# Performance work log

Measured on AMD Instinct MI355X. Metric: run time of the kernel, lower is better.

Reference implementation:

```python
import jax, jax.numpy as jnp
import numpy as np

E, D_IN, D_OUT, T = 8, 2048, 8192, 16384


def setup_inputs() -> dict:
    key = jax.random.key(0)
    k1, k2 = jax.random.split(key, 2)
    inp = jax.random.normal(k1, (T, D_IN), dtype=jnp.float32)
    # kaiming-uniform-ish scale for weight [E, d_out, d_in]
    bound = float(1.0 / np.sqrt(D_IN))
    weight = jax.random.uniform(k2, (E, D_OUT, D_IN), dtype=jnp.float32,
                                minval=-bound, maxval=bound)
    bias = jnp.zeros((E, D_OUT), dtype=jnp.float32)
    # tokens are pre-sorted by expert; equal load here (2048 tokens/expert)
    fwd_expert_count = jnp.full((E,), T // E, dtype=jnp.int32)
    return {"inp": inp, "fwd_expert_count": fwd_expert_count,
            "weight": weight, "bias": bias}


def reference(inp, fwd_expert_count, weight, bias):
    # Grouped GEMM: expert e processes the contiguous slab of
    # fwd_expert_count[e] rows of inp; y = x_e @ W[e].T + b[e].
    counts = np.asarray(fwd_expert_count)          # concrete host ints
    offsets = np.concatenate([[0], np.cumsum(counts)])
    outs = []
    for e in range(counts.shape[0]):
        x_e = inp[offsets[e]:offsets[e + 1]]        # [c_e, d_in]
        outs.append(x_e @ weight[e].T + bias[e])    # [c_e, d_out]
    return jnp.concatenate(outs, axis=0)            # [T, d_out]
```

## Files before the change

### kernel.cpp

```cpp
#include <hip/hip_runtime.h>
#include <stdint.h>

typedef unsigned short u16;
typedef __attribute__((ext_vector_type(8))) short short8;
typedef __attribute__((ext_vector_type(4))) float f32x4;

#define NE   8
#define DIN  2048
#define DOUT 8192
#define NTOK 16384

__device__ __forceinline__ u16 f2bf(float f) {
  uint32_t u = __builtin_bit_cast(uint32_t, f);
  u += 0x7FFFu + ((u >> 16) & 1u);
  return (u16)(u >> 16);
}

__global__ __launch_bounds__(256) void cvt_f32_bf16(const float* __restrict__ src,
                                                    u16* __restrict__ dst, size_t n) {
  size_t i = ((size_t)blockIdx.x * 256 + threadIdx.x) * 8;
  const size_t stride = (size_t)gridDim.x * 256 * 8;
  for (; i < n; i += stride) {
    f32x4 a = *(const f32x4*)(src + i);
    f32x4 b = *(const f32x4*)(src + i + 4);
    short8 o;
    o[0] = (short)f2bf(a[0]); o[1] = (short)f2bf(a[1]);
    o[2] = (short)f2bf(a[2]); o[3] = (short)f2bf(a[3]);
    o[4] = (short)f2bf(b[0]); o[5] = (short)f2bf(b[1]);
    o[6] = (short)f2bf(b[2]); o[7] = (short)f2bf(b[3]);
    *(short8*)(dst + i) = o;
  }
}

#define GLOAD_LDS16(g, l) __builtin_amdgcn_global_load_lds( \
    (const __attribute__((address_space(1))) void*)(g),     \
    (__attribute__((address_space(3))) void*)(l), 16, 0, 0)

__global__ __launch_bounds__(512, 2) void moe_gemm8(
    const u16* __restrict__ Xb, const u16* __restrict__ Wb,
    const int* __restrict__ counts, const float* __restrict__ bias,
    float* __restrict__ C) {
  extern __shared__ u16 sm[];

  const int tid = threadIdx.x;
  const int l = tid & 63;
  const int wid = tid >> 6;
  const int wr = wid >> 2;
  const int wc = wid & 3;

  const int id = blockIdx.x;
  const int swz = (id & 7) * 256 + (id >> 3);
  const int e = swz >> 8;
  const int rem = swz & 255;
  const int tn = rem >> 3;
  const int tm = rem & 7;

  int off = 0;
  for (int i = 0; i < e; ++i) off += counts[i];
  const int row0 = off + tm * 256;
  const int col0 = tn * 256;
  const size_t wbase = (size_t)e * DOUT * DIN + (size_t)col0 * DIN;

  const int rl = l >> 2;
  const int q = (l & 3) ^ ((l >> 3) & 3);
  const int s0 = wid * 2, s1 = s0 + 1;
  const u16* pA0 = Xb + (size_t)(row0 + s0 * 16 + rl) * DIN + q * 8;
  const u16* pA1 = Xb + (size_t)(row0 + s1 * 16 + rl) * DIN + q * 8;
  const u16* pB0 = Wb + wbase + (size_t)(s0 * 16 + rl) * DIN + q * 8;
  const u16* pB1 = Wb + wbase + (size_t)(s1 * 16 + rl) * DIN + q * 8;

  const int f0 = ((l & 15) >> 1) & 3;
  const int gph = (l >> 4) ^ f0;
  const int aoff = (wr * 128 + (l & 15)) * 32 + gph * 8;
  const int boff = (wc * 64 + (l & 15)) * 32 + gph * 8;

  f32x4 acc[8][4] = {};
  short8 a[4], b[4];

#define SMA(buf, kh) (sm + (buf) * 32768 + (kh) * 8192)
#define SMB(buf, kh) (sm + (buf) * 32768 + 16384 + (kh) * 8192)
#define STAGE_A(buf, kt, kh) do { const int ko = (kt) * 64 + (kh) * 32; \
    GLOAD_LDS16(pA0 + ko, SMA(buf, kh) + s0 * 512);                     \
    GLOAD_LDS16(pA1 + ko, SMA(buf, kh) + s1 * 512); } while (0)
#define STAGE_B(buf, kt, kh) do { const int ko = (kt) * 64 + (kh) * 32; \
    GLOAD_LDS16(pB0 + ko, SMB(buf, kh) + s0 * 512);                     \
    GLOAD_LDS16(pB1 + ko, SMB(buf, kh) + s1 * 512); } while (0)
#define RA4(buf, kh, mb) do { _Pragma("unroll") for (int mf = 0; mf < 4; ++mf) \
    a[mf] = *(const short8*)(SMA(buf, kh) + aoff + ((mb) + mf) * 512); } while (0)
#define RB4(buf, kh) do { _Pragma("unroll") for (int nf = 0; nf < 4; ++nf) \
    b[nf] = *(const short8*)(SMB(buf, kh) + boff + nf * 512); } while (0)
#define FENCE() asm volatile("" ::: "memory")
#define BAR() do { FENCE(); __builtin_amdgcn_s_barrier(); FENCE(); } while (0)
#define VMW(N) asm volatile("s_waitcnt vmcnt(" #N ")" ::: "memory")
#define LGKM0() asm volatile("s_waitcnt lgkmcnt(0)" ::: "memory")
#define MMQ(mb) do { __builtin_amdgcn_s_setprio(1);                                \
    _Pragma("unroll") for (int mf = 0; mf < 4; ++mf)                               \
      _Pragma("unroll") for (int nf = 0; nf < 4; ++nf)                             \
        acc[(mb) + mf][nf] =                                                       \
          __builtin_amdgcn_mfma_f32_16x16x32_bf16(a[mf], b[nf], acc[(mb) + mf][nf], 0, 0, 0); \
    __builtin_amdgcn_s_setprio(0); } while (0)

  const int NKT = DIN / 64;

  STAGE_A(0, 0, 0); STAGE_B(0, 0, 0); STAGE_A(0, 0, 1); STAGE_B(0, 0, 1);
  VMW(4);
  BAR();

  for (int kt = 0; kt < NKT; kt += 2) {
#define TILE(cur, nxt, t) do {                                          \
    const bool hn = (t) + 1 < NKT;                                      \
                                   \
    RA4(cur, 0, 0); RB4(cur, 0);                                        \
    if (hn) STAGE_A(nxt, (t) + 1, 0);                                   \
    BAR(); MMQ(0);                                                      \
                         \
    RA4(cur, 0, 4);                                                     \
    if (hn) { STAGE_B(nxt, (t) + 1, 0); VMW(4); } else VMW(0);          \
    BAR(); MMQ(4);                                                      \
                                           \
    RA4(cur, 1, 0); RB4(cur, 1);                                        \
    if (hn) STAGE_A(nxt, (t) + 1, 1);                                   \
    BAR(); MMQ(0);                                                      \
                        \
    RA4(cur, 1, 4);                                                     \
    if (hn) { STAGE_B(nxt, (t) + 1, 1); VMW(4); }                       \
    BAR(); MMQ(4); } while (0)
    TILE(0, 1, kt);
    TILE(1, 0, kt + 1);
#undef TILE
  }

  BAR();
  float* smf = (float*)sm;
  const int cbw = col0 + wc * 64;
  const int r0 = (l >> 4) << 2;
  const f32x4 bv4 = *(const f32x4*)(bias + (size_t)e * DOUT + cbw + (l & 15) * 4);

#pragma unroll
  for (int m = 0; m < 8; ++m) {
    float* eb = smf + (wid * 2 + (m & 1)) * 1088;
#pragma unroll
    for (int n = 0; n < 4; ++n) {
      const int c = n * 16 + (l & 15);
#pragma unroll
      for (int j = 0; j < 4; ++j)
        eb[(r0 + j) * 68 + c] = acc[m][n][j];
    }
    LGKM0();
    const int rbm = row0 + wr * 128 + m * 16;
#pragma unroll
    for (int i = 0; i < 4; ++i) {
      const int row = i * 4 + (l >> 4);
      f32x4 v = *(const f32x4*)(eb + row * 68 + (l & 15) * 4);
      v = v + bv4;
      __builtin_nontemporal_store(
          v, (f32x4*)(C + (size_t)(rbm + row) * DOUT + cbw + (l & 15) * 4));
    }
  }
}

__global__ __launch_bounds__(256) void moe_gemm_fused(
    const float* __restrict__ Xf, const float* __restrict__ Wf,
    const int* __restrict__ counts, const float* __restrict__ bias,
    float* __restrict__ C) {
  __shared__ __align__(16) u16 lds[2][2][128 * 32];

  const int tid = threadIdx.x;
  const int lane = tid & 63;
  const int wid = tid >> 6;
  const int wr = wid >> 1;
  const int wc = wid & 1;

  const int id = blockIdx.x;
  const int swz = (id & 7) * ((int)gridDim.x >> 3) + (id >> 3);
  const int e = swz >> 10;
  const int rem = swz & 1023;
  const int tn = rem >> 4;
  const int tml = rem & 15;

  int off = 0;
  for (int i = 0; i < e; ++i) off += counts[i];
  const int row0 = off + tml * 128;
  const int col0 = tn * 128;
  const size_t wbase = (size_t)e * DOUT * DIN + (size_t)col0 * DIN;

  f32x4 acc[4][4] = {};

  auto stage = [&](int buf, int kt) {
#pragma unroll
    for (int s = 0; s < 2; ++s) {
      int i = s * 256 + tid;
      int r = i >> 2, c = i & 3;
      const float* sa = Xf + (size_t)(row0 + r) * DIN + kt * 32 + c * 8;
      const float* sb = Wf + wbase + (size_t)r * DIN + kt * 32 + c * 8;
      f32x4 a0 = *(const f32x4*)sa;
      f32x4 a1 = *(const f32x4*)(sa + 4);
      f32x4 b0 = *(const f32x4*)sb;
      f32x4 b1 = *(const f32x4*)(sb + 4);
      short8 va, vb;
#pragma unroll
      for (int j = 0; j < 4; ++j) {
        va[j] = (short)f2bf(a0[j]); va[j + 4] = (short)f2bf(a1[j]);
        vb[j] = (short)f2bf(b0[j]); vb[j + 4] = (short)f2bf(b1[j]);
      }
      *(short8*)&lds[buf][0][i * 8] = va;
      *(short8*)&lds[buf][1][i * 8] = vb;
    }
  };

  auto compute = [&](int buf) {
    const int kc = lane >> 4;
    const int rr = lane & 15;
    short8 a[4], b[4];
    const u16* lA = lds[buf][0];
    const u16* lB = lds[buf][1];
#pragma unroll
    for (int m = 0; m < 4; ++m)
      a[m] = *(const short8*)(lA + (wr * 64 + m * 16 + rr) * 32 + kc * 8);
#pragma unroll
    for (int n = 0; n < 4; ++n)
      b[n] = *(const short8*)(lB + (wc * 64 + n * 16 + rr) * 32 + kc * 8);
#pragma unroll
    for (int m = 0; m < 4; ++m)
#pragma unroll
      for (int n = 0; n < 4; ++n)
        acc[m][n] = __builtin_amdgcn_mfma_f32_16x16x32_bf16(a[m], b[n], acc[m][n], 0, 0, 0);
  };

  stage(0, 0);
  for (int kt = 0; kt < DIN / 32; ++kt) {
    __syncthreads();
    if (kt + 1 < DIN / 32) stage((kt + 1) & 1, kt + 1);
    compute(kt & 1);
  }

  const int rbase = row0 + wr * 64;
  const int cbase = col0 + wc * 64;
#pragma unroll
  for (int n = 0; n < 4; ++n) {
    const int col = cbase + n * 16 + (lane & 15);
    const float bv = bias[e * DOUT + col];
#pragma unroll
    for (int m = 0; m < 4; ++m) {
      const int r0 = rbase + m * 16 + (lane >> 4) * 4;
#pragma unroll
      for (int j = 0; j < 4; ++j)
        C[(size_t)(r0 + j) * DOUT + col] = acc[m][n][j] + bv;
    }
  }
}

extern "C" void kernel_launch(void* const* d_in, const int* in_sizes, int n_in,
                              void* d_out, int out_size, void* d_ws, size_t ws_size,
                              hipStream_t stream) {
  const float* inp = (const float*)d_in[0];
  const int* counts = (const int*)d_in[1];
  const float* weight = (const float*)d_in[2];
  const float* bias = (const float*)d_in[3];
  float* out = (float*)d_out;

  const size_t nx = (size_t)NTOK * DIN;
  const size_t nw = (size_t)NE * DOUT * DIN;
  const size_t need = (nx + nw) * sizeof(u16);

  if (ws_size >= need) {
    u16* xb = (u16*)d_ws;
    u16* wb = xb + nx;
    cvt_f32_bf16<<<2048, 256, 0, stream>>>(inp, xb, nx);
    cvt_f32_bf16<<<4096, 256, 0, stream>>>(weight, wb, nw);
    const int grid = (NTOK / 256) * (DOUT / 256);
    moe_gemm8<<<grid, 512, 131072, stream>>>(xb, wb, counts, bias, out);
  } else {
    const int grid = (NTOK / 128) * (DOUT / 128);
    moe_gemm_fused<<<grid, 256, 0, stream>>>(inp, weight, counts, bias, out);
  }
}
```

Before: 730.5 us.

## Fuse weight fp32-to-bf16 conversion into GEMM B-tile LDS reads

Drops the separate kernel that converts the 512MB fp32 weight tensor to bf16. The GEMM now stages fp32 weight tiles straight into LDS and converts them to bf16 when reading fragments. The K-step is cut to 32 with a simpler two-phase pipeline and less LDS per block. This removes a full read-and-write pass over the weights, but the GEMM now reads twice the B bytes per tile, does conversion ALU work inside the MFMA loop, and waits on all loads every K-step.

```diff
diff --git a/kernel.cpp b/kernel.cpp
--- a/kernel.cpp
+++ b/kernel.cpp
@@ -37,10 +37,11 @@
     (__attribute__((address_space(3))) void*)(l), 16, 0, 0)
 
 __global__ __launch_bounds__(512, 2) void moe_gemm8(
-    const u16* __restrict__ Xb, const u16* __restrict__ Wb,
+    const u16* __restrict__ Xb, const float* __restrict__ Wf,
     const int* __restrict__ counts, const float* __restrict__ bias,
     float* __restrict__ C) {
   extern __shared__ u16 sm[];
+  float* smBf = (float*)(sm + 16384);
 
   const int tid = threadIdx.x;
   const int l = tid & 63;
@@ -62,33 +63,47 @@
   const size_t wbase = (size_t)e * DOUT * DIN + (size_t)col0 * DIN;
 
   const int rl = l >> 2;
-  const int q = (l & 3) ^ ((l >> 3) & 3);
+  const int qA = (l & 3) ^ ((l >> 3) & 3);
   const int s0 = wid * 2, s1 = s0 + 1;
-  const u16* pA0 = Xb + (size_t)(row0 + s0 * 16 + rl) * DIN + q * 8;
-  const u16* pA1 = Xb + (size_t)(row0 + s1 * 16 + rl) * DIN + q * 8;
-  const u16* pB0 = Wb + wbase + (size_t)(s0 * 16 + rl) * DIN + q * 8;
-  const u16* pB1 = Wb + wbase + (size_t)(s1 * 16 + rl) * DIN + q * 8;
-
-  const int f0 = ((l & 15) >> 1) & 3;
-  const int gph = (l >> 4) ^ f0;
+  const u16* pA0 = Xb + (size_t)(row0 + s0 * 16 + rl) * DIN + qA * 8;
+  const u16* pA1 = Xb + (size_t)(row0 + s1 * 16 + rl) * DIN + qA * 8;
+
+  const int rj = l >> 3;
+  const int qB = (l & 7) ^ rj;
+  const int sb = wid * 4;
+  const float* pB0 = Wf + wbase + (size_t)((sb + 0) * 8 + rj) * DIN + qB * 4;
+  const float* pB1 = Wf + wbase + (size_t)((sb + 1) * 8 + rj) * DIN + qB * 4;
+  const float* pB2 = Wf + wbase + (size_t)((sb + 2) * 8 + rj) * DIN + qB * 4;
+  const float* pB3 = Wf + wbase + (size_t)((sb + 3) * 8 + rj) * DIN + qB * 4;
+
+  const int gph = (l >> 4) ^ (((l & 15) >> 1) & 3);
   const int aoff = (wr * 128 + (l & 15)) * 32 + gph * 8;
-  const int boff = (wc * 64 + (l & 15)) * 32 + gph * 8;
+  const int h = l >> 4;
+  const int bo0 = (wc * 64 + (l & 15)) * 32 + ((2 * h) ^ (l & 7)) * 4;
+  const int bo1 = (wc * 64 + (l & 15)) * 32 + ((2 * h + 1) ^ (l & 7)) * 4;
 
   f32x4 acc[8][4] = {};
   short8 a[4], b[4];
 
-#define SMA(buf, kh) (sm + (buf) * 32768 + (kh) * 8192)
-#define SMB(buf, kh) (sm + (buf) * 32768 + 16384 + (kh) * 8192)
-#define STAGE_A(buf, kt, kh) do { const int ko = (kt) * 64 + (kh) * 32; \
-    GLOAD_LDS16(pA0 + ko, SMA(buf, kh) + s0 * 512);                     \
-    GLOAD_LDS16(pA1 + ko, SMA(buf, kh) + s1 * 512); } while (0)
-#define STAGE_B(buf, kt, kh) do { const int ko = (kt) * 64 + (kh) * 32; \
-    GLOAD_LDS16(pB0 + ko, SMB(buf, kh) + s0 * 512);                     \
-    GLOAD_LDS16(pB1 + ko, SMB(buf, kh) + s1 * 512); } while (0)
-#define RA4(buf, kh, mb) do { _Pragma("unroll") for (int mf = 0; mf < 4; ++mf) \
-    a[mf] = *(const short8*)(SMA(buf, kh) + aoff + ((mb) + mf) * 512); } while (0)
-#define RB4(buf, kh) do { _Pragma("unroll") for (int nf = 0; nf < 4; ++nf) \
-    b[nf] = *(const short8*)(SMB(buf, kh) + boff + nf * 512); } while (0)
+#define SMA(buf) (sm + (buf) * 8192)
+#define SMB(buf) (smBf + (buf) * 8192)
+#define STAGE_A(buf, kt) do { const int ko = (kt) * 32;          \
+    GLOAD_LDS16(pA0 + ko, SMA(buf) + s0 * 512);                  \
+    GLOAD_LDS16(pA1 + ko, SMA(buf) + s1 * 512); } while (0)
+#define STAGE_B(buf, kt) do { const int ko = (kt) * 32;          \
+    GLOAD_LDS16(pB0 + ko, SMB(buf) + (sb + 0) * 256);            \
+    GLOAD_LDS16(pB1 + ko, SMB(buf) + (sb + 1) * 256);            \
+    GLOAD_LDS16(pB2 + ko, SMB(buf) + (sb + 2) * 256);            \
+    GLOAD_LDS16(pB3 + ko, SMB(buf) + (sb + 3) * 256); } while (0)
+#define RA4(buf, mb) do { _Pragma("unroll") for (int mf = 0; mf < 4; ++mf) \
+    a[mf] = *(const short8*)(SMA(buf) + aoff + ((mb) + mf) * 512); } while (0)
+#define RB4F(buf) do { _Pragma("unroll") for (int nf = 0; nf < 4; ++nf) {  \
+    f32x4 v0 = *(const f32x4*)(SMB(buf) + bo0 + nf * 512);                 \
+    f32x4 v1 = *(const f32x4*)(SMB(buf) + bo1 + nf * 512);                 \
+    short8 t_;                                                             \
+    _Pragma("unroll") for (int j = 0; j < 4; ++j) {                        \
+      t_[j] = (short)f2bf(v0[j]); t_[4 + j] = (short)f2bf(v1[j]); }        \
+    b[nf] = t_; } } while (0)
 #define FENCE() asm volatile("" ::: "memory")
 #define BAR() do { FENCE(); __builtin_amdgcn_s_barrier(); FENCE(); } while (0)
 #define VMW(N) asm volatile("s_waitcnt vmcnt(" #N ")" ::: "memory")
@@ -100,30 +115,22 @@
           __builtin_amdgcn_mfma_f32_16x16x32_bf16(a[mf], b[nf], acc[(mb) + mf][nf], 0, 0, 0); \
     __builtin_amdgcn_s_setprio(0); } while (0)
 
-  const int NKT = DIN / 64;
-
-  STAGE_A(0, 0, 0); STAGE_B(0, 0, 0); STAGE_A(0, 0, 1); STAGE_B(0, 0, 1);
-  VMW(4);
+  const int NKT = DIN / 32;
+
+  STAGE_A(0, 0); STAGE_B(0, 0);
+  VMW(0);
   BAR();
 
   for (int kt = 0; kt < NKT; kt += 2) {
 #define TILE(cur, nxt, t) do {                                          \
     const bool hn = (t) + 1 < NKT;                                      \
-                                   \
-    RA4(cur, 0, 0); RB4(cur, 0);                                        \
-    if (hn) STAGE_A(nxt, (t) + 1, 0);                                   \
+     \
+    if (hn) { STAGE_A(nxt, (t) + 1); STAGE_B(nxt, (t) + 1); }           \
+    RA4(cur, 0); RB4F(cur);                                             \
     BAR(); MMQ(0);                                                      \
-                         \
-    RA4(cur, 0, 4);                                                     \
-    if (hn) { STAGE_B(nxt, (t) + 1, 0); VMW(4); } else VMW(0);          \
-    BAR(); MMQ(4);                                                      \
-                                           \
-    RA4(cur, 1, 0); RB4(cur, 1);                                        \
-    if (hn) STAGE_A(nxt, (t) + 1, 1);                                   \
-    BAR(); MMQ(0);                                                      \
-                        \
-    RA4(cur, 1, 4);                                                     \
-    if (hn) { STAGE_B(nxt, (t) + 1, 1); VMW(4); }                       \
+            \
+    RA4(cur, 4);                                                        \
+    VMW(0);                                                             \
     BAR(); MMQ(4); } while (0)
     TILE(0, 1, kt);
     TILE(1, 0, kt + 1);
@@ -260,16 +267,13 @@
   float* out = (float*)d_out;
 
   const size_t nx = (size_t)NTOK * DIN;
-  const size_t nw = (size_t)NE * DOUT * DIN;
-  const size_t need = (nx + nw) * sizeof(u16);
+  const size_t need = nx * sizeof(u16);
 
   if (ws_size >= need) {
     u16* xb = (u16*)d_ws;
-    u16* wb = xb + nx;
     cvt_f32_bf16<<<2048, 256, 0, stream>>>(inp, xb, nx);
-    cvt_f32_bf16<<<4096, 256, 0, stream>>>(weight, wb, nw);
     const int grid = (NTOK / 256) * (DOUT / 256);
-    moe_gemm8<<<grid, 512, 131072, stream>>>(xb, wb, counts, bias, out);
+    moe_gemm8<<<grid, 512, 98304, stream>>>(xb, weight, counts, bias, out);
   } else {
     const int grid = (NTOK / 128) * (DOUT / 128);
     moe_gemm_fused<<<grid, 256, 0, stream>>>(inp, weight, counts, bias, out);
```

New measurement: 918.9 us. +25.8%, slower.

## Shrink GEMM tile to 256x128 with smaller LDS and higher occupancy

Applied to the files above, without the earlier changes.

The bf16 grouped GEMM tile goes from 256x256 to 256x128, with 8 waves arranged 4x2 and 64x64 accumulators per wave. The K step drops from 64 to 32 with a simpler double-buffered pipeline, LDS falls from 128KB to 48KB, and launch bounds ask for 4 blocks per CU. This raises occupancy and latency hiding but lowers arithmetic intensity, since each block reloads A tiles twice as often and runs twice as many blocks.

```diff
diff --git a/kernel.cpp b/kernel.cpp
--- a/kernel.cpp
+++ b/kernel.cpp
@@ -36,7 +36,7 @@
     (const __attribute__((address_space(1))) void*)(g),     \
     (__attribute__((address_space(3))) void*)(l), 16, 0, 0)
 
-__global__ __launch_bounds__(512, 2) void moe_gemm8(
+__global__ __launch_bounds__(512, 4) void moe_gemm8(
     const u16* __restrict__ Xb, const u16* __restrict__ Wb,
     const int* __restrict__ counts, const float* __restrict__ bias,
     float* __restrict__ C) {
@@ -45,20 +45,20 @@
   const int tid = threadIdx.x;
   const int l = tid & 63;
   const int wid = tid >> 6;
-  const int wr = wid >> 2;
-  const int wc = wid & 3;
+  const int wr = wid >> 1;
+  const int wc = wid & 1;
 
   const int id = blockIdx.x;
-  const int swz = (id & 7) * 256 + (id >> 3);
-  const int e = swz >> 8;
-  const int rem = swz & 255;
+  const int swz = (id & 7) * 512 + (id >> 3);
+  const int e = swz >> 9;
+  const int rem = swz & 511;
   const int tn = rem >> 3;
   const int tm = rem & 7;
 
   int off = 0;
   for (int i = 0; i < e; ++i) off += counts[i];
   const int row0 = off + tm * 256;
-  const int col0 = tn * 256;
+  const int col0 = tn * 128;
   const size_t wbase = (size_t)e * DOUT * DIN + (size_t)col0 * DIN;
 
   const int rl = l >> 2;
@@ -66,79 +66,69 @@
   const int s0 = wid * 2, s1 = s0 + 1;
   const u16* pA0 = Xb + (size_t)(row0 + s0 * 16 + rl) * DIN + q * 8;
   const u16* pA1 = Xb + (size_t)(row0 + s1 * 16 + rl) * DIN + q * 8;
-  const u16* pB0 = Wb + wbase + (size_t)(s0 * 16 + rl) * DIN + q * 8;
-  const u16* pB1 = Wb + wbase + (size_t)(s1 * 16 + rl) * DIN + q * 8;
-
-  const int f0 = ((l & 15) >> 1) & 3;
-  const int gph = (l >> 4) ^ f0;
-  const int aoff = (wr * 128 + (l & 15)) * 32 + gph * 8;
+  const u16* pB0 = Wb + wbase + (size_t)(wid * 16 + rl) * DIN + q * 8;
+
+  const int gph = (l >> 4) ^ (((l & 15) >> 1) & 3);
+  const int aoff = (wr * 64 + (l & 15)) * 32 + gph * 8;
   const int boff = (wc * 64 + (l & 15)) * 32 + gph * 8;
 
-  f32x4 acc[8][4] = {};
+  f32x4 acc[4][4] = {};
   short8 a[4], b[4];
 
-#define SMA(buf, kh) (sm + (buf) * 32768 + (kh) * 8192)
-#define SMB(buf, kh) (sm + (buf) * 32768 + 16384 + (kh) * 8192)
-#define STAGE_A(buf, kt, kh) do { const int ko = (kt) * 64 + (kh) * 32; \
-    GLOAD_LDS16(pA0 + ko, SMA(buf, kh) + s0 * 512);                     \
-    GLOAD_LDS16(pA1 + ko, SMA(buf, kh) + s1 * 512); } while (0)
-#define STAGE_B(buf, kt, kh) do { const int ko = (kt) * 64 + (kh) * 32; \
-    GLOAD_LDS16(pB0 + ko, SMB(buf, kh) + s0 * 512);                     \
-    GLOAD_LDS16(pB1 + ko, SMB(buf, kh) + s1 * 512); } while (0)
-#define RA4(buf, kh, mb) do { _Pragma("unroll") for (int mf = 0; mf < 4; ++mf) \
-    a[mf] = *(const short8*)(SMA(buf, kh) + aoff + ((mb) + mf) * 512); } while (0)
-#define RB4(buf, kh) do { _Pragma("unroll") for (int nf = 0; nf < 4; ++nf) \
-    b[nf] = *(const short8*)(SMB(buf, kh) + boff + nf * 512); } while (0)
+#define SMA(buf) (sm + (buf) * 8192)
+#define SMB(buf) (sm + 16384 + (buf) * 4096)
+#define STAGE(buf, kt) do { const int ko = (kt) * 32;      \
+    GLOAD_LDS16(pA0 + ko, SMA(buf) + s0 * 512);            \
+    GLOAD_LDS16(pA1 + ko, SMA(buf) + s1 * 512);            \
+    GLOAD_LDS16(pB0 + ko, SMB(buf) + wid * 512); } while (0)
+#define RA4(buf) do { _Pragma("unroll") for (int mf = 0; mf < 4; ++mf) \
+    a[mf] = *(const short8*)(SMA(buf) + aoff + mf * 512); } while (0)
+#define RB4(buf) do { _Pragma("unroll") for (int nf = 0; nf < 4; ++nf) \
+    b[nf] = *(const short8*)(SMB(buf) + boff + nf * 512); } while (0)
 #define FENCE() asm volatile("" ::: "memory")
 #define BAR() do { FENCE(); __builtin_amdgcn_s_barrier(); FENCE(); } while (0)
 #define VMW(N) asm volatile("s_waitcnt vmcnt(" #N ")" ::: "memory")
 #define LGKM0() asm volatile("s_waitcnt lgkmcnt(0)" ::: "memory")
-#define MMQ(mb) do { __builtin_amdgcn_s_setprio(1);                                \
+#define MM16() do { __builtin_amdgcn_s_setprio(1);                                 \
     _Pragma("unroll") for (int mf = 0; mf < 4; ++mf)                               \
       _Pragma("unroll") for (int nf = 0; nf < 4; ++nf)                             \
-        acc[(mb) + mf][nf] =                                                       \
-          __builtin_amdgcn_mfma_f32_16x16x32_bf16(a[mf], b[nf], acc[(mb) + mf][nf], 0, 0, 0); \
+        acc[mf][nf] =                                                              \
+          __builtin_amdgcn_mfma_f32_16x16x32_bf16(a[mf], b[nf], acc[mf][nf], 0, 0, 0); \
     __builtin_amdgcn_s_setprio(0); } while (0)
 
-  const int NKT = DIN / 64;
-
-  STAGE_A(0, 0, 0); STAGE_B(0, 0, 0); STAGE_A(0, 0, 1); STAGE_B(0, 0, 1);
-  VMW(4);
+  const int NKT = DIN / 32;
+
+  STAGE(0, 0); STAGE(1, 1);
+  VMW(3);
   BAR();
 
   for (int kt = 0; kt < NKT; kt += 2) {
 #define TILE(cur, nxt, t) do {                                          \
-    const bool hn = (t) + 1 < NKT;                                      \
-                                   \
-    RA4(cur, 0, 0); RB4(cur, 0);                                        \
-    if (hn) STAGE_A(nxt, (t) + 1, 0);                                   \
-    BAR(); MMQ(0);                                                      \
-                         \
-    RA4(cur, 0, 4);                                                     \
-    if (hn) { STAGE_B(nxt, (t) + 1, 0); VMW(4); } else VMW(0);          \
-    BAR(); MMQ(4);                                                      \
-                                           \
-    RA4(cur, 1, 0); RB4(cur, 1);                                        \
-    if (hn) STAGE_A(nxt, (t) + 1, 1);                                   \
-    BAR(); MMQ(0);                                                      \
-                        \
-    RA4(cur, 1, 4);                                                     \
-    if (hn) { STAGE_B(nxt, (t) + 1, 1); VMW(4); }                       \
-    BAR(); MMQ(4); } while (0)
+    const bool h1 = (t) + 1 < NKT;                                      \
+    const bool h2 = (t) + 2 < NKT;                                      \
+                            \
+    RA4(cur); RB4(cur);                                                 \
+    LGKM0(); BAR();         \
+    if (h2) STAGE(cur, (t) + 2);     \
+    MM16();                                                             \
+    if (h2) VMW(3);                 \
+    else if (h1) VMW(0);       \
+    BAR();                                       \
+    } while (0)
     TILE(0, 1, kt);
     TILE(1, 0, kt + 1);
 #undef TILE
   }
 
-  BAR();
   float* smf = (float*)sm;
   const int cbw = col0 + wc * 64;
   const int r0 = (l >> 4) << 2;
   const f32x4 bv4 = *(const f32x4*)(bias + (size_t)e * DOUT + cbw + (l & 15) * 4);
-
-#pragma unroll
-  for (int m = 0; m < 8; ++m) {
-    float* eb = smf + (wid * 2 + (m & 1)) * 1088;
+  float* eb = smf + wid * 1088;
+
+#pragma unroll
+  for (int m = 0; m < 4; ++m) {
+    if (m) LGKM0();
 #pragma unroll
     for (int n = 0; n < 4; ++n) {
       const int c = n * 16 + (l & 15);
@@ -147,7 +137,7 @@
         eb[(r0 + j) * 68 + c] = acc[m][n][j];
     }
     LGKM0();
-    const int rbm = row0 + wr * 128 + m * 16;
+    const int rbm = row0 + wr * 64 + m * 16;
 #pragma unroll
     for (int i = 0; i < 4; ++i) {
       const int row = i * 4 + (l >> 4);
@@ -268,8 +258,8 @@
     u16* wb = xb + nx;
     cvt_f32_bf16<<<2048, 256, 0, stream>>>(inp, xb, nx);
     cvt_f32_bf16<<<4096, 256, 0, stream>>>(weight, wb, nw);
-    const int grid = (NTOK / 256) * (DOUT / 256);
-    moe_gemm8<<<grid, 512, 131072, stream>>>(xb, wb, counts, bias, out);
+    const int grid = (NTOK / 256) * (DOUT / 128);
+    moe_gemm8<<<grid, 512, 49152, stream>>>(xb, wb, counts, bias, out);
   } else {
     const int grid = (NTOK / 128) * (DOUT / 128);
     moe_gemm_fused<<<grid, 256, 0, stream>>>(inp, weight, counts, bias, out);
```

Result: slower. 790.0 us (+8.1%).
